# Kernel optimization log

Measured on AMD Instinct MI355X. Metric: run time of the kernel, lower is better.

Reference implementation:

```python
import jax, jax.numpy as jnp
import numpy as np

N = 8192
F_IN = 512
F_OUT = 64
ALPHA = 0.2  # LeakyReLU negative slope
NEG_INF = -9e15


def setup_inputs() -> dict:
    key = jax.random.key(0)
    k1, k2, k3, k4 = jax.random.split(key, 4)
    inp = jax.random.normal(k1, (N, F_IN), dtype=jnp.float32)
    adj = jax.random.randint(k2, (N, N), 0, 2, dtype=jnp.int32)
    W = jax.random.normal(k3, (F_IN, F_OUT), dtype=jnp.float32) * 0.05
    a = jax.random.normal(k4, (2 * F_OUT, 1), dtype=jnp.float32) * 0.05
    return {"inp": inp, "adj": adj, "W": W, "a": a}


def reference(inp, adj, W, a):
    # h = W(inp): [N, F_OUT]
    h = inp @ W
    # a([h_i || h_j]) decomposes exactly into a1.h_i + a2.h_j, avoiding the
    # [N*N, 2F] concat tensor while computing identical math.
    f1 = h @ a[:F_OUT]        # [N, 1] source-node term
    f2 = h @ a[F_OUT:]        # [N, 1] target-node term
    e = jax.nn.leaky_relu(f1 + f2.T, negative_slope=ALPHA)  # [N, N]
    masked = jnp.where(adj > 0, e, jnp.float32(NEG_INF))
    attention = jax.nn.softmax(masked, axis=1)  # dropout is no-op at inference
    h_prime = attention @ h   # [N, F_OUT]
    return jax.nn.elu(h_prime)  # concat=True branch
```

## Files before the change

### kernel.cpp

```cpp
#include <hip/hip_runtime.h>

#define NN   8192
#define FIN  512
#define FOUT 64
#define KHALF 4096

typedef __attribute__((ext_vector_type(8)))  short short8;
typedef __attribute__((ext_vector_type(4)))  float floatx4;
typedef __attribute__((ext_vector_type(16))) float floatx16;

__device__ __forceinline__ unsigned f2bf_u(float f) {
  union { float f; unsigned u; } v; v.f = f;
  return (v.u + 0x7fffu + ((v.u >> 16) & 1u)) >> 16;
}
__device__ __forceinline__ unsigned pack2(float a, float b) {
  return f2bf_u(a) | (f2bf_u(b) << 16);
}
__device__ __forceinline__ short8 as_s8(int4 v) {
  union { int4 a; short8 b; } u; u.a = v; return u.b;
}

__global__ __launch_bounds__(256) void k1_gemm_h(
    const float* __restrict__ inp, const float* __restrict__ W,
    const float* __restrict__ a,
    float* __restrict__ f1, float* __restrict__ f2,
    unsigned short* __restrict__ hT)
{
  __shared__ unsigned short at[32][72];
  __shared__ unsigned short wt[64][72];
  __shared__ float hsm[32][65];
  __shared__ float alds[2 * FOUT];

  const int tid   = threadIdx.x;
  const int rbase = blockIdx.x * 32;
  if (tid < 2 * FOUT) alds[tid] = a[tid];

  const int lane = tid & 63;
  const int wv   = tid >> 6;
  const int l15  = lane & 15;
  const int q    = lane >> 4;
  const int mi   = wv & 1;
  const int ni0  = (wv >> 1) * 2;

  const int r_a  = tid >> 3;
  const int k8   = (tid & 7) * 8;
  const int n_w  = tid & 63;
  const int kb_w = (tid >> 6) * 16;

  floatx4 acc0 = {0.f, 0.f, 0.f, 0.f};
  floatx4 acc1 = {0.f, 0.f, 0.f, 0.f};

  for (int kk0 = 0; kk0 < FIN; kk0 += 64) {
    __syncthreads();
    const float* ap = inp + (rbase + r_a) * FIN + kk0 + k8;
    float4 v0 = *(const float4*)ap;
    float4 v1 = *(const float4*)(ap + 4);
    *(uint4*)&at[r_a][k8] = make_uint4(pack2(v0.x, v0.y), pack2(v0.z, v0.w),
                                       pack2(v1.x, v1.y), pack2(v1.z, v1.w));
#pragma unroll
    for (int kk2 = 0; kk2 < 16; ++kk2)
      wt[n_w][kb_w + kk2] = (unsigned short)f2bf_u(W[(kk0 + kb_w + kk2) * FOUT + n_w]);
    __syncthreads();
#pragma unroll
    for (int ks = 0; ks < 2; ++ks) {
      short8 af = *(const short8*)&at[mi * 16 + l15][ks * 32 + q * 8];
      short8 b0 = *(const short8*)&wt[ni0 * 16 + l15][ks * 32 + q * 8];
      short8 b1 = *(const short8*)&wt[(ni0 + 1) * 16 + l15][ks * 32 + q * 8];
      acc0 = __builtin_amdgcn_mfma_f32_16x16x32_bf16(af, b0, acc0, 0, 0, 0);
      acc1 = __builtin_amdgcn_mfma_f32_16x16x32_bf16(af, b1, acc1, 0, 0, 0);
    }
  }

  {
    const int m0 = mi * 16 + q * 4;
    const int i0 = rbase + m0;
    {
      const int n = ni0 * 16 + l15;
#pragma unroll
      for (int rg = 0; rg < 4; ++rg) hsm[m0 + rg][n] = acc0[rg];
      *(uint2*)&hT[n * NN + i0] = make_uint2(pack2(acc0[0], acc0[1]),
                                             pack2(acc0[2], acc0[3]));
    }
    {
      const int n = (ni0 + 1) * 16 + l15;
#pragma unroll
      for (int rg = 0; rg < 4; ++rg) hsm[m0 + rg][n] = acc1[rg];
      *(uint2*)&hT[n * NN + i0] = make_uint2(pack2(acc1[0], acc1[1]),
                                             pack2(acc1[2], acc1[3]));
    }
  }
  __syncthreads();
  if (tid < 32) {
    float s1 = 0.f, s2 = 0.f;
#pragma unroll 8
    for (int c = 0; c < FOUT; ++c) {
      float hv = hsm[tid][c];
      s1 += hv * alds[c];
      s2 += hv * alds[FOUT + c];
    }
    f1[rbase + tid] = s1;
    f2[rbase + tid] = s2;
  }
}

__device__ __forceinline__ short8 mkw(const int4 A0, const int4 A1,
                                      const float4 F0, const float4 F1,
                                      const float f1v, float& lsum) {
  float e, w0, w1, w2, w3, w4, w5, w6, w7;
  e = f1v + F0.x; e = fmaxf(e, 0.2f * e); w0 = A0.x ? __expf(e) : 0.f;
  e = f1v + F0.y; e = fmaxf(e, 0.2f * e); w1 = A0.y ? __expf(e) : 0.f;
  e = f1v + F0.z; e = fmaxf(e, 0.2f * e); w2 = A0.z ? __expf(e) : 0.f;
  e = f1v + F0.w; e = fmaxf(e, 0.2f * e); w3 = A0.w ? __expf(e) : 0.f;
  e = f1v + F1.x; e = fmaxf(e, 0.2f * e); w4 = A1.x ? __expf(e) : 0.f;
  e = f1v + F1.y; e = fmaxf(e, 0.2f * e); w5 = A1.y ? __expf(e) : 0.f;
  e = f1v + F1.z; e = fmaxf(e, 0.2f * e); w6 = A1.z ? __expf(e) : 0.f;
  e = f1v + F1.w; e = fmaxf(e, 0.2f * e); w7 = A1.w ? __expf(e) : 0.f;
  lsum += ((w0 + w1) + (w2 + w3)) + ((w4 + w5) + (w6 + w7));
  uint4 u = make_uint4(pack2(w0, w1), pack2(w2, w3), pack2(w4, w5), pack2(w6, w7));
  union { uint4 a; short8 b; } c; c.a = u; return c.b;
}

__global__ __launch_bounds__(256, 2) void k2_attn(
    const int* __restrict__ adj,
    const float* __restrict__ f1g, const float* __restrict__ f2g,
    const unsigned short* __restrict__ hT,
    float* __restrict__ part, float* __restrict__ lpart)
{
  __shared__ float pbuf[4][2048];
  __shared__ float lsw[4][32];

  const int tid   = threadIdx.x;
  const int wv    = tid >> 6;
  const int lane  = tid & 63;
  const int i32   = lane & 31;
  const int hi    = lane >> 5;
  const int rbase = (blockIdx.x >> 1) * 32;
  const int kh    = blockIdx.x & 1;
  const int kbase = kh * KHALF + wv * 32 + hi * 8;

  const int*            ap  = adj + (size_t)(rbase + i32) * NN + kbase;
  const float*          fp  = f2g + kbase;
  const unsigned short* h0p = hT + (size_t)i32 * NN + kbase;
  const unsigned short* h1p = h0p + (size_t)32 * NN;
  const float f1v = f1g[rbase + i32];

  floatx16 acc0 = {0,0,0,0,0,0,0,0,0,0,0,0,0,0,0,0};
  floatx16 acc1 = {0,0,0,0,0,0,0,0,0,0,0,0,0,0,0,0};
  float lsum = 0.f;

  int4  A0  = *(const int4*)(ap);       int4  A1  = *(const int4*)(ap + 4);
  int4  A2  = *(const int4*)(ap + 16);  int4  A3  = *(const int4*)(ap + 20);
  float4 F0 = *(const float4*)(fp);     float4 F1 = *(const float4*)(fp + 4);
  float4 F2 = *(const float4*)(fp + 16);float4 F3 = *(const float4*)(fp + 20);
  int4  H00 = *(const int4*)(h0p);      int4  H01 = *(const int4*)(h0p + 16);
  int4  H10 = *(const int4*)(h1p);      int4  H11 = *(const int4*)(h1p + 16);

  for (int it = 0; it < KHALF / 128; ++it) {
    const int nk = (it < KHALF / 128 - 1) ? (it + 1) * 128 : 0;
    int4  nA0 = *(const int4*)(ap + nk);       int4  nA1 = *(const int4*)(ap + nk + 4);
    int4  nA2 = *(const int4*)(ap + nk + 16);  int4  nA3 = *(const int4*)(ap + nk + 20);
    float4 nF0 = *(const float4*)(fp + nk);    float4 nF1 = *(const float4*)(fp + nk + 4);
    float4 nF2 = *(const float4*)(fp + nk + 16);float4 nF3 = *(const float4*)(fp + nk + 20);
    int4  nH00 = *(const int4*)(h0p + nk);     int4  nH01 = *(const int4*)(h0p + nk + 16);
    int4  nH10 = *(const int4*)(h1p + nk);     int4  nH11 = *(const int4*)(h1p + nk + 16);

    short8 b0 = mkw(A0, A1, F0, F1, f1v, lsum);
    acc0 = __builtin_amdgcn_mfma_f32_32x32x16_bf16(as_s8(H00), b0, acc0, 0, 0, 0);
    acc1 = __builtin_amdgcn_mfma_f32_32x32x16_bf16(as_s8(H10), b0, acc1, 0, 0, 0);
    short8 b1 = mkw(A2, A3, F2, F3, f1v, lsum);
    acc0 = __builtin_amdgcn_mfma_f32_32x32x16_bf16(as_s8(H01), b1, acc0, 0, 0, 0);
    acc1 = __builtin_amdgcn_mfma_f32_32x32x16_bf16(as_s8(H11), b1, acc1, 0, 0, 0);

    A0 = nA0; A1 = nA1; A2 = nA2; A3 = nA3;
    F0 = nF0; F1 = nF1; F2 = nF2; F3 = nF3;
    H00 = nH00; H01 = nH01; H10 = nH10; H11 = nH11;
  }

  lsum += __shfl_xor(lsum, 32, 64);
  if (lane < 32) lsw[wv][i32] = lsum;

#pragma unroll
  for (int rg = 0; rg < 16; ++rg) {
    const int m = (rg & 3) + 8 * (rg >> 2) + 4 * hi;
    pbuf[wv][i32 * 64 + m]      = acc0[rg];
    pbuf[wv][i32 * 64 + 32 + m] = acc1[rg];
  }
  __syncthreads();

  const int e0 = tid * 8;
  const int irow = rbase + (e0 >> 6);
  const int f0c  = e0 & 63;
  float* dst = part + ((size_t)kh * NN + irow) * 64 + f0c;
#pragma unroll
  for (int c = 0; c < 2; ++c) {
    float4 s = *(const float4*)&pbuf[0][e0 + c * 4];
    float4 s1 = *(const float4*)&pbuf[1][e0 + c * 4];
    float4 s2 = *(const float4*)&pbuf[2][e0 + c * 4];
    float4 s3 = *(const float4*)&pbuf[3][e0 + c * 4];
    s.x += s1.x + s2.x + s3.x; s.y += s1.y + s2.y + s3.y;
    s.z += s1.z + s2.z + s3.z; s.w += s1.w + s2.w + s3.w;
    *(float4*)(dst + c * 4) = s;
  }
  if (tid < 32)
    lpart[(size_t)kh * NN + rbase + tid] =
        lsw[0][tid] + lsw[1][tid] + lsw[2][tid] + lsw[3][tid];
}

__global__ __launch_bounds__(256) void k3_combine(
    const float* __restrict__ part, const float* __restrict__ lpart,
    float* __restrict__ out)
{
  const int gid = blockIdx.x * 256 + threadIdx.x;
  const int i = gid >> 4;
  const int c = (gid & 15) * 4;
  const float inv = 1.f / (lpart[i] + lpart[NN + i]);
  float4 p0 = *(const float4*)(part + (size_t)i * 64 + c);
  float4 p1 = *(const float4*)(part + ((size_t)NN + i) * 64 + c);
  float4 v;
  v.x = (p0.x + p1.x) * inv; v.x = (v.x > 0.f) ? v.x : (__expf(v.x) - 1.f);
  v.y = (p0.y + p1.y) * inv; v.y = (v.y > 0.f) ? v.y : (__expf(v.y) - 1.f);
  v.z = (p0.z + p1.z) * inv; v.z = (v.z > 0.f) ? v.z : (__expf(v.z) - 1.f);
  v.w = (p0.w + p1.w) * inv; v.w = (v.w > 0.f) ? v.w : (__expf(v.w) - 1.f);
  *(float4*)(out + (size_t)i * 64 + c) = v;
}

extern "C" void kernel_launch(void* const* d_in, const int* in_sizes, int n_in,
                              void* d_out, int out_size, void* d_ws, size_t ws_size,
                              hipStream_t stream) {
  (void)in_sizes; (void)n_in; (void)out_size; (void)ws_size;
  const float* inp = (const float*)d_in[0];
  const int*   adj = (const int*)d_in[1];
  const float* W   = (const float*)d_in[2];
  const float* a   = (const float*)d_in[3];
  float* out = (float*)d_out;

  float* f1 = (float*)d_ws;
  float* f2 = f1 + NN;
  unsigned short* hT = (unsigned short*)(f2 + NN);
  float* part  = (float*)(hT + (size_t)FOUT * NN);
  float* lpart = part + 2 * (size_t)NN * FOUT;

  k1_gemm_h<<<NN / 32, 256, 0, stream>>>(inp, W, a, f1, f2, hT);
  k2_attn<<<(NN / 32) * 2, 256, 0, stream>>>(adj, f1, f2, hT, part, lpart);
  k3_combine<<<NN * FOUT / 4 / 256, 256, 0, stream>>>(part, lpart, out);
}
```

Measured before the change: 399.7 us.

## Restructure attention kernel to 16-row tiles with LDS-staged weights and 16x16 MFMA

The attention kernel now handles 16 rows per block instead of 32. Each thread computes masked exp weights for contiguous 16-column chunks of adj and writes them as bf16 into a double-buffered LDS tile. Waves then read A fragments from LDS and hT fragments from global memory to feed 16x16x32 bf16 MFMAs over all 64 output features. The goal is fully coalesced adj reads with no redundant exp work, plus a doubled grid and occupancy hint of 4 for more latency hiding. In exchange it adds a __syncthreads per iteration, and hT is now re-read by twice as many blocks.

Measured after the change: 401.1 us. No clear change (+0.4%).

```diff
diff --git a/kernel.cpp b/kernel.cpp
--- a/kernel.cpp
+++ b/kernel.cpp
@@ -7,7 +7,6 @@
 
 typedef __attribute__((ext_vector_type(8)))  short short8;
 typedef __attribute__((ext_vector_type(4)))  float floatx4;
-typedef __attribute__((ext_vector_type(16))) float floatx16;
 
 __device__ __forceinline__ unsigned f2bf_u(float f) {
   union { float f; unsigned u; } v; v.f = f;
@@ -15,9 +14,6 @@
 }
 __device__ __forceinline__ unsigned pack2(float a, float b) {
   return f2bf_u(a) | (f2bf_u(b) << 16);
-}
-__device__ __forceinline__ short8 as_s8(int4 v) {
-  union { int4 a; short8 b; } u; u.a = v; return u.b;
 }
 
 __global__ __launch_bounds__(256) void k1_gemm_h(
@@ -103,7 +99,7 @@
   }
 }
 
-__device__ __forceinline__ short8 mkw(const int4 A0, const int4 A1,
+__device__ __forceinline__ uint4 mkw8(const int4 A0, const int4 A1,
                                       const float4 F0, const float4 F1,
                                       const float f1v, float& lsum) {
   float e, w0, w1, w2, w3, w4, w5, w6, w7;
@@ -116,94 +112,105 @@
   e = f1v + F1.z; e = fmaxf(e, 0.2f * e); w6 = A1.z ? __expf(e) : 0.f;
   e = f1v + F1.w; e = fmaxf(e, 0.2f * e); w7 = A1.w ? __expf(e) : 0.f;
   lsum += ((w0 + w1) + (w2 + w3)) + ((w4 + w5) + (w6 + w7));
-  uint4 u = make_uint4(pack2(w0, w1), pack2(w2, w3), pack2(w4, w5), pack2(w6, w7));
-  union { uint4 a; short8 b; } c; c.a = u; return c.b;
-}
-
-__global__ __launch_bounds__(256, 2) void k2_attn(
+  return make_uint4(pack2(w0, w1), pack2(w2, w3), pack2(w4, w5), pack2(w6, w7));
+}
+
+__global__ __launch_bounds__(256, 4) void k2_attn(
     const int* __restrict__ adj,
     const float* __restrict__ f1g, const float* __restrict__ f2g,
     const unsigned short* __restrict__ hT,
     float* __restrict__ part, float* __restrict__ lpart)
 {
-  __shared__ float pbuf[4][2048];
-  __shared__ float lsw[4][32];
+  __shared__ unsigned short wlds[2][16][264];
+  __shared__ float pbuf[4][1024];
+  __shared__ float lred[16][17];
 
   const int tid   = threadIdx.x;
   const int wv    = tid >> 6;
   const int lane  = tid & 63;
-  const int i32   = lane & 31;
-  const int hi    = lane >> 5;
-  const int rbase = (blockIdx.x >> 1) * 32;
+  const int l15   = lane & 15;
+  const int q     = lane >> 4;
+  const int rbase = (blockIdx.x >> 1) * 16;
   const int kh    = blockIdx.x & 1;
-  const int kbase = kh * KHALF + wv * 32 + hi * 8;
-
-  const int*            ap  = adj + (size_t)(rbase + i32) * NN + kbase;
-  const float*          fp  = f2g + kbase;
-  const unsigned short* h0p = hT + (size_t)i32 * NN + kbase;
-  const unsigned short* h1p = h0p + (size_t)32 * NN;
-  const float f1v = f1g[rbase + i32];
-
-  floatx16 acc0 = {0,0,0,0,0,0,0,0,0,0,0,0,0,0,0,0};
-  floatx16 acc1 = {0,0,0,0,0,0,0,0,0,0,0,0,0,0,0,0};
+  const int kb    = kh * KHALF;
+
+  const int r = tid >> 4;
+  const int c = tid & 15;
+
+  const int*   ap = adj + (size_t)(rbase + r) * NN + kb + c * 16;
+  const float* fp = f2g + kb + c * 16;
+  const float f1v = f1g[rbase + r];
+
+  const unsigned short* hp = hT + (size_t)l15 * NN + kb + wv * 64 + q * 8;
+
+  floatx4 acc[4];
+#pragma unroll
+  for (int ft = 0; ft < 4; ++ft) acc[ft] = (floatx4){0.f, 0.f, 0.f, 0.f};
   float lsum = 0.f;
 
-  int4  A0  = *(const int4*)(ap);       int4  A1  = *(const int4*)(ap + 4);
-  int4  A2  = *(const int4*)(ap + 16);  int4  A3  = *(const int4*)(ap + 20);
-  float4 F0 = *(const float4*)(fp);     float4 F1 = *(const float4*)(fp + 4);
-  float4 F2 = *(const float4*)(fp + 16);float4 F3 = *(const float4*)(fp + 20);
-  int4  H00 = *(const int4*)(h0p);      int4  H01 = *(const int4*)(h0p + 16);
-  int4  H10 = *(const int4*)(h1p);      int4  H11 = *(const int4*)(h1p + 16);
-
-  for (int it = 0; it < KHALF / 128; ++it) {
-    const int nk = (it < KHALF / 128 - 1) ? (it + 1) * 128 : 0;
-    int4  nA0 = *(const int4*)(ap + nk);       int4  nA1 = *(const int4*)(ap + nk + 4);
-    int4  nA2 = *(const int4*)(ap + nk + 16);  int4  nA3 = *(const int4*)(ap + nk + 20);
-    float4 nF0 = *(const float4*)(fp + nk);    float4 nF1 = *(const float4*)(fp + nk + 4);
-    float4 nF2 = *(const float4*)(fp + nk + 16);float4 nF3 = *(const float4*)(fp + nk + 20);
-    int4  nH00 = *(const int4*)(h0p + nk);     int4  nH01 = *(const int4*)(h0p + nk + 16);
-    int4  nH10 = *(const int4*)(h1p + nk);     int4  nH11 = *(const int4*)(h1p + nk + 16);
-
-    short8 b0 = mkw(A0, A1, F0, F1, f1v, lsum);
-    acc0 = __builtin_amdgcn_mfma_f32_32x32x16_bf16(as_s8(H00), b0, acc0, 0, 0, 0);
-    acc1 = __builtin_amdgcn_mfma_f32_32x32x16_bf16(as_s8(H10), b0, acc1, 0, 0, 0);
-    short8 b1 = mkw(A2, A3, F2, F3, f1v, lsum);
-    acc0 = __builtin_amdgcn_mfma_f32_32x32x16_bf16(as_s8(H01), b1, acc0, 0, 0, 0);
-    acc1 = __builtin_amdgcn_mfma_f32_32x32x16_bf16(as_s8(H11), b1, acc1, 0, 0, 0);
-
+  int4 A0 = *(const int4*)(ap);
+  int4 A1 = *(const int4*)(ap + 4);
+  int4 A2 = *(const int4*)(ap + 8);
+  int4 A3 = *(const int4*)(ap + 12);
+
+  for (int it = 0; it < KHALF / 256; ++it) {
+    const int nk = (it < KHALF / 256 - 1) ? (it + 1) * 256 : 0;
+    int4 nA0 = *(const int4*)(ap + nk);
+    int4 nA1 = *(const int4*)(ap + nk + 4);
+    int4 nA2 = *(const int4*)(ap + nk + 8);
+    int4 nA3 = *(const int4*)(ap + nk + 12);
+
+    const int b = it & 1;
+    {
+      float4 F0 = *(const float4*)(fp + it * 256);
+      float4 F1 = *(const float4*)(fp + it * 256 + 4);
+      *(uint4*)&wlds[b][r][c * 16] = mkw8(A0, A1, F0, F1, f1v, lsum);
+    }
+    {
+      float4 F2 = *(const float4*)(fp + it * 256 + 8);
+      float4 F3 = *(const float4*)(fp + it * 256 + 12);
+      *(uint4*)&wlds[b][r][c * 16 + 8] = mkw8(A2, A3, F2, F3, f1v, lsum);
+    }
+    __syncthreads();
+    const unsigned short* hit = hp + it * 256;
+#pragma unroll
+    for (int ks = 0; ks < 2; ++ks) {
+      short8 af = *(const short8*)&wlds[b][l15][wv * 64 + ks * 32 + q * 8];
+#pragma unroll
+      for (int ft = 0; ft < 4; ++ft) {
+        short8 bf = *(const short8*)(hit + ks * 32 + (size_t)ft * 16 * NN);
+        acc[ft] = __builtin_amdgcn_mfma_f32_16x16x32_bf16(af, bf, acc[ft], 0, 0, 0);
+      }
+    }
     A0 = nA0; A1 = nA1; A2 = nA2; A3 = nA3;
-    F0 = nF0; F1 = nF1; F2 = nF2; F3 = nF3;
-    H00 = nH00; H01 = nH01; H10 = nH10; H11 = nH11;
-  }
-
-  lsum += __shfl_xor(lsum, 32, 64);
-  if (lane < 32) lsw[wv][i32] = lsum;
-
-#pragma unroll
-  for (int rg = 0; rg < 16; ++rg) {
-    const int m = (rg & 3) + 8 * (rg >> 2) + 4 * hi;
-    pbuf[wv][i32 * 64 + m]      = acc0[rg];
-    pbuf[wv][i32 * 64 + 32 + m] = acc1[rg];
-  }
+  }
+
+#pragma unroll
+  for (int ft = 0; ft < 4; ++ft)
+#pragma unroll
+    for (int rg = 0; rg < 4; ++rg)
+      pbuf[wv][(q * 4 + rg) * 64 + ft * 16 + l15] = acc[ft][rg];
+  lred[r][c] = lsum;
   __syncthreads();
 
-  const int e0 = tid * 8;
-  const int irow = rbase + (e0 >> 6);
-  const int f0c  = e0 & 63;
-  float* dst = part + ((size_t)kh * NN + irow) * 64 + f0c;
-#pragma unroll
-  for (int c = 0; c < 2; ++c) {
-    float4 s = *(const float4*)&pbuf[0][e0 + c * 4];
-    float4 s1 = *(const float4*)&pbuf[1][e0 + c * 4];
-    float4 s2 = *(const float4*)&pbuf[2][e0 + c * 4];
-    float4 s3 = *(const float4*)&pbuf[3][e0 + c * 4];
-    s.x += s1.x + s2.x + s3.x; s.y += s1.y + s2.y + s3.y;
-    s.z += s1.z + s2.z + s3.z; s.w += s1.w + s2.w + s3.w;
-    *(float4*)(dst + c * 4) = s;
-  }
-  if (tid < 32)
-    lpart[(size_t)kh * NN + rbase + tid] =
-        lsw[0][tid] + lsw[1][tid] + lsw[2][tid] + lsw[3][tid];
+  {
+    const int e0 = tid * 4;
+    const int row = e0 >> 6;
+    const int f0 = e0 & 63;
+    float4 s0 = *(const float4*)&pbuf[0][e0];
+    float4 s1 = *(const float4*)&pbuf[1][e0];
+    float4 s2 = *(const float4*)&pbuf[2][e0];
+    float4 s3 = *(const float4*)&pbuf[3][e0];
+    s0.x += s1.x + s2.x + s3.x; s0.y += s1.y + s2.y + s3.y;
+    s0.z += s1.z + s2.z + s3.z; s0.w += s1.w + s2.w + s3.w;
+    *(float4*)(part + ((size_t)kh * NN + rbase + row) * 64 + f0) = s0;
+  }
+  if (tid < 16) {
+    float s = 0.f;
+#pragma unroll
+    for (int i = 0; i < 16; ++i) s += lred[tid][i];
+    lpart[(size_t)kh * NN + rbase + tid] = s;
+  }
 }
 
 __global__ __launch_bounds__(256) void k3_combine(
@@ -241,6 +248,6 @@
   float* lpart = part + 2 * (size_t)NN * FOUT;
 
   k1_gemm_h<<<NN / 32, 256, 0, stream>>>(inp, W, a, f1, f2, hT);
-  k2_attn<<<(NN / 32) * 2, 256, 0, stream>>>(adj, f1, f2, hT, part, lpart);
+  k2_attn<<<(NN / 16) * 2, 256, 0, stream>>>(adj, f1, f2, hT, part, lpart);
   k3_combine<<<NN * FOUT / 4 / 256, 256, 0, stream>>>(part, lpart, out);
 }
```
